# Optimization experiments

Measured on AMD Instinct MI355X. Metric: run time of the kernel, lower is better.

The kernel has to match this reference:

```python
import jax, jax.numpy as jnp
import numpy as np

N, L, S, D, HD, FC = 4, 2048, 2048, 256, 256, 8  # batch, query len, source len, in_depth, hidden_depth, heads
EPS = 1e-12  # F.normalize eps


def setup_inputs() -> dict:
    key = jax.random.key(0)
    ks = jax.random.split(key, 8)
    sc = 0.05
    return {
        "x0": jax.random.normal(ks[0], (N, L, D), jnp.float32),
        "x1": jax.random.normal(ks[1], (N, S, D), jnp.float32),
        "W0": jax.random.normal(ks[2], (D, HD), jnp.float32) * sc,
        "b0": jax.random.normal(ks[3], (HD,), jnp.float32) * sc,
        "W1": jax.random.normal(ks[4], (D, 2 * HD), jnp.float32) * sc,
        "b1": jax.random.normal(ks[5], (2 * HD,), jnp.float32) * sc,
        "Wm": jax.random.normal(ks[6], (HD, D), jnp.float32) * sc,
        "bm": jax.random.normal(ks[7], (D,), jnp.float32) * sc,
        "alpha": jnp.ones((1,), jnp.float32),
        "beta": jnp.zeros((1,), jnp.float32),
    }


def _l2norm(x):
    # F.normalize(dim=2): x / max(||x||, eps)
    return x / jnp.maximum(jnp.linalg.norm(x, axis=2, keepdims=True), EPS)


def reference(x0, x1, W0, b0, W1, b1, Wm, bm, alpha, beta):
    n, l, _ = x0.shape
    s = x1.shape[1]
    fc = FC
    m = n * fc
    # projections + head split: 'n l (fc c) -> (n fc) l c'
    x0p = (x0 @ W0 + b0).reshape(n, l, fc, -1).transpose(0, 2, 1, 3).reshape(m, l, -1)
    x1p = (x1 @ W1 + b1).reshape(n, s, fc, -1).transpose(0, 2, 1, 3).reshape(m, s, -1)
    x1_point, x1_value = jnp.split(x1p, 2, axis=2)  # each (m, s, c)
    # cosine similarity (m, l, s)
    sim = jnp.einsum('mlc,msc->mls', _l2norm(x0p), _l2norm(x1_point))
    sim = jax.nn.sigmoid(alpha * sim + beta)
    max_val = jnp.max(sim, axis=2)              # (m, l)
    max_idx = jnp.argmax(sim, axis=2)           # (m, l)
    gathered = jnp.take_along_axis(x1_value, max_idx[:, :, None], axis=1)  # (m, l, c)
    new_x0 = max_val[:, :, None] * gathered
    # '(n fc) l c -> n l (fc c)'
    new_x0 = new_x0.reshape(n, fc, l, -1).transpose(0, 2, 1, 3).reshape(n, l, -1)
    return new_x0 @ Wm + bm
```

## Files before the change

kernel.cpp:

```cpp
#include <hip/hip_runtime.h>
#include <hip/hip_bf16.h>
#include <cmath>

#define NB   4
#define LQ   2048
#define SK   2048
#define DD   256
#define HD   256
#define FC   8
#define CH   32
#define MHEAD 32

#define MARGIN 0.0085f
#define CAP    12

typedef float f32x16 __attribute__((ext_vector_type(16)));
typedef short bf16x8 __attribute__((ext_vector_type(8)));
typedef unsigned short ushort8v __attribute__((ext_vector_type(8)));

__device__ inline unsigned short f32_to_bf16_bits(float v) {
    __hip_bfloat16 b = __float2bfloat16(v);
    return __builtin_bit_cast(unsigned short, b);
}
__device__ inline unsigned int ord_encode(float v) {
    unsigned int u = __float_as_uint(v);
    return (u & 0x80000000u) ? ~u : (u | 0x80000000u);
}
__device__ inline float ord_decode(unsigned int e) {
    unsigned int u = (e & 0x80000000u) ? (e & 0x7fffffffu) : ~e;
    return __uint_as_float(u);
}

#define MFMA32(a, b, c) __builtin_amdgcn_mfma_f32_32x32x16_bf16(a, b, c, 0, 0, 0)

template<int EPI>
__global__ __launch_bounds__(256)
void gemm_bias_kernel(const float* __restrict__ A, const float* __restrict__ B,
                      const float* __restrict__ bias,
                      float* __restrict__ C0, float* __restrict__ C1,
                      int M, int N, int K)
{
    __shared__ float As[16][68];
    __shared__ float Bs[16][64];
    const int tx = threadIdx.x & 15;
    const int ty = threadIdx.x >> 4;
    const int bm = blockIdx.y * 64;
    const int bn = blockIdx.x * 64;
    float acc[4][4] = {};

    for (int k0 = 0; k0 < K; k0 += 16) {
        {
            const int row = threadIdx.x >> 2;
            const int kq  = (threadIdx.x & 3) << 2;
            const float4 a4 = *(const float4*)&A[(size_t)(bm + row) * K + k0 + kq];
            As[kq + 0][row] = a4.x;
            As[kq + 1][row] = a4.y;
            As[kq + 2][row] = a4.z;
            As[kq + 3][row] = a4.w;
            const int kr = threadIdx.x >> 4;
            const int nq = (threadIdx.x & 15) << 2;
            *(float4*)&Bs[kr][nq] = *(const float4*)&B[(size_t)(k0 + kr) * N + bn + nq];
        }
        __syncthreads();
        #pragma unroll
        for (int kk = 0; kk < 16; ++kk) {
            const float4 a4 = *(const float4*)&As[kk][ty << 2];
            const float4 b4 = *(const float4*)&Bs[kk][tx << 2];
            const float av[4] = {a4.x, a4.y, a4.z, a4.w};
            const float bv[4] = {b4.x, b4.y, b4.z, b4.w};
            #pragma unroll
            for (int i = 0; i < 4; ++i)
                #pragma unroll
                for (int j = 0; j < 4; ++j)
                    acc[i][j] = fmaf(av[i], bv[j], acc[i][j]);
        }
        __syncthreads();
    }

    #pragma unroll
    for (int i = 0; i < 4; ++i) {
        const int row = bm + (ty << 2) + i;
        #pragma unroll
        for (int j = 0; j < 4; ++j) {
            const int col = bn + (tx << 2) + j;
            const float v = acc[i][j] + bias[col];
            if (EPI == 0) {
                C0[(size_t)row * N + col] = v;
            } else if (EPI == 1) {
                const int n = row >> 11, l = row & 2047;
                const int f = col >> 5,  c = col & 31;
                C0[((((size_t)n * FC + f) * LQ) + l) * CH + c] = v;
            } else {
                const int n = row >> 11, s = row & 2047;
                const int f = col >> 6,  c64 = col & 63;
                float* dst = (c64 < CH) ? C0 : C1;
                dst[((((size_t)n * FC + f) * SK) + s) * CH + (c64 & 31)] = v;
            }
        }
    }
}

__global__ __launch_bounds__(256)
void norm_hi_kernel(float* __restrict__ x, unsigned short* __restrict__ dhi,
                    int nrows, const float* __restrict__ alpha)
{
    const int r = blockIdx.x * blockDim.x + threadIdx.x;
    if (r >= nrows) return;
    float* p = x + (size_t)r * CH;
    float4 v[8];
    float ss = 0.f;
    #pragma unroll
    for (int i = 0; i < 8; ++i) {
        v[i] = *(const float4*)(p + i * 4);
        ss = fmaf(v[i].x, v[i].x, ss);
        ss = fmaf(v[i].y, v[i].y, ss);
        ss = fmaf(v[i].z, v[i].z, ss);
        ss = fmaf(v[i].w, v[i].w, ss);
    }
    float sgn = 1.f;
    if (alpha) sgn = (alpha[0] < 0.f) ? -1.f : 1.f;
    const float inv = sgn / fmaxf(sqrtf(ss), 1e-12f);

    ushort8v hb[4];
    #pragma unroll
    for (int i = 0; i < 8; ++i) {
        float4 w;
        w.x = v[i].x * inv; w.y = v[i].y * inv;
        w.z = v[i].z * inv; w.w = v[i].w * inv;
        *(float4*)(p + i * 4) = w;
        hb[i >> 1][(i & 1) * 4 + 0] = f32_to_bf16_bits(w.x);
        hb[i >> 1][(i & 1) * 4 + 1] = f32_to_bf16_bits(w.y);
        hb[i >> 1][(i & 1) * 4 + 2] = f32_to_bf16_bits(w.z);
        hb[i >> 1][(i & 1) * 4 + 3] = f32_to_bf16_bits(w.w);
    }
    #pragma unroll
    for (int i = 0; i < 4; ++i)
        *(ushort8v*)(dhi + (size_t)r * CH + i * 8) = hb[i];
}

__global__ __launch_bounds__(256, 4)
void maxpass_kernel(const unsigned short* __restrict__ qhi,
                    const unsigned short* __restrict__ khi,
                    unsigned int* __restrict__ maxhh_u)
{
    const int b    = blockIdx.x;
    const int sc   = b & 3;
    const int qb   = (b >> 2) & 15;
    const int h    = b >> 6;
    const int wave = threadIdx.x >> 6;
    const int lane = threadIdx.x & 63;
    const int qbase = qb * 128 + wave * 32;
    const int col   = lane & 31;
    const int g8    = (lane >> 5) * 8;

    const size_t qoff = ((size_t)h * LQ + qbase + col) * CH + g8;
    const bf16x8 ah0 = *(const bf16x8*)(qhi + qoff);
    const bf16x8 ah1 = *(const bf16x8*)(qhi + qoff + 16);

    const unsigned short* kh = khi + ((size_t)h * SK + sc * 512) * CH;
    const size_t koff = (size_t)col * CH + g8;

    float maxv[16];
    #pragma unroll
    for (int r = 0; r < 16; ++r) maxv[r] = -INFINITY;

    bf16x8 t0a = *(const bf16x8*)(kh + koff);
    bf16x8 t0b = *(const bf16x8*)(kh + koff + 16);
    bf16x8 t1a = *(const bf16x8*)(kh + koff + 32 * CH);
    bf16x8 t1b = *(const bf16x8*)(kh + koff + 32 * CH + 16);

    for (int sb = 0; sb < 16; sb += 2) {
        const bf16x8 c0a = t0a, c0b = t0b, c1a = t1a, c1b = t1b;
        if (sb + 2 < 16) {
            const size_t o = koff + (size_t)(sb + 2) * 32 * CH;
            t0a = *(const bf16x8*)(kh + o);
            t0b = *(const bf16x8*)(kh + o + 16);
            t1a = *(const bf16x8*)(kh + o + 32 * CH);
            t1b = *(const bf16x8*)(kh + o + 32 * CH + 16);
        }
        f32x16 c = {0.f, 0.f, 0.f, 0.f, 0.f, 0.f, 0.f, 0.f,
                    0.f, 0.f, 0.f, 0.f, 0.f, 0.f, 0.f, 0.f};
        c = MFMA32(ah0, c0a, c);
        c = MFMA32(ah1, c0b, c);
        #pragma unroll
        for (int r = 0; r < 16; ++r) maxv[r] = fmaxf(maxv[r], c[r]);
        f32x16 d = {0.f, 0.f, 0.f, 0.f, 0.f, 0.f, 0.f, 0.f,
                    0.f, 0.f, 0.f, 0.f, 0.f, 0.f, 0.f, 0.f};
        d = MFMA32(ah0, c1a, d);
        d = MFMA32(ah1, c1b, d);
        #pragma unroll
        for (int r = 0; r < 16; ++r) maxv[r] = fmaxf(maxv[r], d[r]);
    }

    #pragma unroll
    for (int r = 0; r < 16; ++r) {
        float v = maxv[r];
        #pragma unroll
        for (int m = 16; m >= 1; m >>= 1)
            v = fmaxf(v, __shfl_xor(v, m, 64));
        maxv[r] = v;
    }
    if (col == 0) {
        const int rbase = h * LQ + qbase + 4 * (lane >> 5);
        #pragma unroll
        for (int r = 0; r < 16; ++r)
            atomicMax(&maxhh_u[rbase + (r & 3) + 8 * (r >> 2)], ord_encode(maxv[r]));
    }
}

__global__ __launch_bounds__(256, 4)
void candpass_kernel(const unsigned short* __restrict__ qhi,
                     const unsigned short* __restrict__ khi,
                     const unsigned int* __restrict__ maxhh_u,
                     int* __restrict__ cnt, int* __restrict__ cand)
{
    const int b    = blockIdx.x;
    const int sc   = b & 3;
    const int qb   = (b >> 2) & 15;
    const int h    = b >> 6;
    const int wave = threadIdx.x >> 6;
    const int lane = threadIdx.x & 63;
    const int qbase = qb * 128 + wave * 32;
    const int col   = lane & 31;
    const int g8    = (lane >> 5) * 8;

    const size_t qoff = ((size_t)h * LQ + qbase + col) * CH + g8;
    const bf16x8 ah0 = *(const bf16x8*)(qhi + qoff);
    const bf16x8 ah1 = *(const bf16x8*)(qhi + qoff + 16);

    int   rows[16];
    float thr[16];
    {
        const int rbase = h * LQ + qbase + 4 * (lane >> 5);
        #pragma unroll
        for (int r = 0; r < 16; ++r) {
            rows[r] = rbase + (r & 3) + 8 * (r >> 2);
            thr[r]  = ord_decode(maxhh_u[rows[r]]) - MARGIN;
        }
    }

    const unsigned short* kh = khi + ((size_t)h * SK + sc * 512) * CH;
    const size_t koff = (size_t)col * CH + g8;
    const int sbase = sc * 512;

    bf16x8 t0a = *(const bf16x8*)(kh + koff);
    bf16x8 t0b = *(const bf16x8*)(kh + koff + 16);
    bf16x8 t1a = *(const bf16x8*)(kh + koff + 32 * CH);
    bf16x8 t1b = *(const bf16x8*)(kh + koff + 32 * CH + 16);

    for (int sb = 0; sb < 16; sb += 2) {
        const bf16x8 c0a = t0a, c0b = t0b, c1a = t1a, c1b = t1b;
        if (sb + 2 < 16) {
            const size_t o = koff + (size_t)(sb + 2) * 32 * CH;
            t0a = *(const bf16x8*)(kh + o);
            t0b = *(const bf16x8*)(kh + o + 16);
            t1a = *(const bf16x8*)(kh + o + 32 * CH);
            t1b = *(const bf16x8*)(kh + o + 32 * CH + 16);
        }
        f32x16 c = {0.f, 0.f, 0.f, 0.f, 0.f, 0.f, 0.f, 0.f,
                    0.f, 0.f, 0.f, 0.f, 0.f, 0.f, 0.f, 0.f};
        c = MFMA32(ah0, c0a, c);
        c = MFMA32(ah1, c0b, c);
        f32x16 d = {0.f, 0.f, 0.f, 0.f, 0.f, 0.f, 0.f, 0.f,
                    0.f, 0.f, 0.f, 0.f, 0.f, 0.f, 0.f, 0.f};
        d = MFMA32(ah0, c1a, d);
        d = MFMA32(ah1, c1b, d);
        const int s0 = sbase + sb * 32 + col;
        #pragma unroll
        for (int r = 0; r < 16; ++r) {
            if (c[r] >= thr[r]) {
                const int slot = atomicAdd(&cnt[rows[r]], 1);
                if (slot < CAP) cand[(size_t)rows[r] * CAP + slot] = s0;
            }
            if (d[r] >= thr[r]) {
                const int slot = atomicAdd(&cnt[rows[r]], 1);
                if (slot < CAP) cand[(size_t)rows[r] * CAP + slot] = s0 + 32;
            }
        }
    }
}

__global__ __launch_bounds__(256)
void refine_gather_kernel(const float* __restrict__ qn,
                          const float* __restrict__ kn,
                          const int* __restrict__ cnt, const int* __restrict__ cand,
                          const float* __restrict__ xv,
                          const float* __restrict__ alpha, const float* __restrict__ beta,
                          unsigned short* __restrict__ nxb)
{
    const int r = blockIdx.x * blockDim.x + threadIdx.x;
    const int h = r >> 11, l = r & 2047;

    float qr[CH];
    #pragma unroll
    for (int i = 0; i < 8; ++i) {
        const float4 v = *(const float4*)(qn + (size_t)r * CH + i * 4);
        qr[i * 4 + 0] = v.x; qr[i * 4 + 1] = v.y;
        qr[i * 4 + 2] = v.z; qr[i * 4 + 3] = v.w;
    }

    int m = cnt[r];
    if (m > CAP) m = CAP;
    float best = -INFINITY;
    int   bidx = 0x7fffffff;
    for (int j = 0; j < m; ++j) {
        const int s = cand[(size_t)r * CAP + j];
        const float4* k4 = (const float4*)(kn + ((size_t)h * SK + s) * CH);
        float p = 0.f;
        #pragma unroll
        for (int c = 0; c < 8; ++c) {
            const float4 kv = k4[c];
            p = fmaf(qr[c * 4 + 0], kv.x, p);
            p = fmaf(qr[c * 4 + 1], kv.y, p);
            p = fmaf(qr[c * 4 + 2], kv.z, p);
            p = fmaf(qr[c * 4 + 3], kv.w, p);
        }
        if (p > best || (p == best && s < bidx)) { best = p; bidx = s; }
    }
    if (bidx == 0x7fffffff) bidx = 0;

    const float a = alpha[0], be = beta[0];
    float tv;
    int idx = bidx;
    if (a == 0.f) { idx = 0; tv = be; }
    else          { tv = fmaf(fabsf(a), best, be); }
    float val;
    if (tv >= 0.f) val = 1.f / (1.f + expf(-tv));
    else           { const float e = expf(tv); val = e / (1.f + e); }

    const float4* vr = (const float4*)(xv + ((size_t)h * SK + idx) * CH);
    const int n = h >> 3, f = h & 7;
    unsigned short* out = nxb + (((size_t)n * LQ + l) * (FC * CH)) + f * CH;
    #pragma unroll
    for (int i = 0; i < 8; ++i) {
        const float4 w = vr[i];
        ushort8v o;
        o[0] = f32_to_bf16_bits(w.x * val);
        o[1] = f32_to_bf16_bits(w.y * val);
        o[2] = f32_to_bf16_bits(w.z * val);
        o[3] = f32_to_bf16_bits(w.w * val);
        *(unsigned long long*)(out + i * 4) = __builtin_bit_cast(unsigned long long,
            *(const ulong1*)&o);
    }
}

__global__ __launch_bounds__(256)
void wmprep_kernel(const float* __restrict__ Wm, unsigned short* __restrict__ wm_s)
{
    const int i = blockIdx.x * 256 + threadIdx.x;
    const int k = i >> 8, n = i & 255;
    wm_s[(k >> 4) * 4096 + n * 16 + (k & 15)] = f32_to_bf16_bits(Wm[k * 256 + n]);
}

__global__ __launch_bounds__(256)
void gemm_out_mfma_kernel(const unsigned short* __restrict__ nxb,
                          const unsigned short* __restrict__ wm_s,
                          const float* __restrict__ bm, float* __restrict__ out)
{
    const int wave = threadIdx.x >> 6;
    const int lane = threadIdx.x & 63;
    const int idx  = blockIdx.x * 4 + wave;
    const int mt   = idx >> 3;
    const int nt   = idx & 7;
    const int col  = lane & 31;
    const int g8   = (lane >> 5) * 8;

    const unsigned short* aptr = nxb + (size_t)(mt * 32 + col) * 256 + g8;
    const unsigned short* bptr = wm_s + nt * 32 * 16 + col * 16 + g8;

    f32x16 acc = {0.f, 0.f, 0.f, 0.f, 0.f, 0.f, 0.f, 0.f,
                  0.f, 0.f, 0.f, 0.f, 0.f, 0.f, 0.f, 0.f};
    #pragma unroll 4
    for (int kc = 0; kc < 16; ++kc) {
        const bf16x8 a = *(const bf16x8*)(aptr + kc * 16);
        const bf16x8 bfr = *(const bf16x8*)(bptr + (size_t)kc * 4096);
        acc = MFMA32(a, bfr, acc);
    }

    const int n0 = nt * 32;
    const float bias = bm[n0 + col];
    #pragma unroll
    for (int r = 0; r < 16; ++r) {
        const int row = mt * 32 + (r & 3) + 8 * (r >> 2) + 4 * (lane >> 5);
        out[(size_t)row * 256 + n0 + col] = acc[r] + bias;
    }
}

extern "C" void kernel_launch(void* const* d_in, const int* in_sizes, int n_in,
                              void* d_out, int out_size, void* d_ws, size_t ws_size,
                              hipStream_t stream)
{
    const float* x0 = (const float*)d_in[0];
    const float* x1 = (const float*)d_in[1];
    const float* W0 = (const float*)d_in[2];
    const float* b0 = (const float*)d_in[3];
    const float* W1 = (const float*)d_in[4];
    const float* b1 = (const float*)d_in[5];
    const float* Wm = (const float*)d_in[6];
    const float* bm = (const float*)d_in[7];
    const float* alpha = (const float*)d_in[8];
    const float* beta  = (const float*)d_in[9];
    float* out = (float*)d_out;

    char* ws = (char*)d_ws;
    const size_t MB = 1024ull * 1024ull;
    float* x0q = (float*)(ws + 0);
    float* x1k = (float*)(ws + 8 * MB);
    float* x1v = (float*)(ws + 16 * MB);
    unsigned short* qhi = (unsigned short*)(ws + 24 * MB);
    unsigned short* khi = (unsigned short*)(ws + 28 * MB);
    unsigned int* maxhh_u = (unsigned int*)(ws + 32 * MB);
    int* cnt  = (int*)(ws + 32 * MB + 256 * 1024);
    int* cand = (int*)(ws + 32 * MB + 512 * 1024);
    unsigned short* wm_s = (unsigned short*)(ws + 32 * MB + 3584 * 1024);
    unsigned short* nxb  = (unsigned short*)(ws + 24 * MB);

    const int Mrows = NB * LQ;

    gemm_bias_kernel<1><<<dim3(HD / 64, Mrows / 64), 256, 0, stream>>>(
        x0, W0, b0, x0q, nullptr, Mrows, HD, DD);
    gemm_bias_kernel<2><<<dim3(2 * HD / 64, Mrows / 64), 256, 0, stream>>>(
        x1, W1, b1, x1k, x1v, Mrows, 2 * HD, DD);
    wmprep_kernel<<<256, 256, 0, stream>>>(Wm, wm_s);
    norm_hi_kernel<<<(MHEAD * LQ) / 256, 256, 0, stream>>>(x0q, qhi, MHEAD * LQ, alpha);
    norm_hi_kernel<<<(MHEAD * SK) / 256, 256, 0, stream>>>(x1k, khi, MHEAD * SK, nullptr);
    hipMemsetAsync(maxhh_u, 0, (size_t)MHEAD * LQ * 4, stream);
    hipMemsetAsync(cnt, 0, (size_t)MHEAD * LQ * 4, stream);
    maxpass_kernel<<<2048, 256, 0, stream>>>(qhi, khi, maxhh_u);
    candpass_kernel<<<2048, 256, 0, stream>>>(qhi, khi, maxhh_u, cnt, cand);
    refine_gather_kernel<<<(MHEAD * LQ) / 256, 256, 0, stream>>>(
        x0q, x1k, cnt, cand, x1v, alpha, beta, nxb);
    gemm_out_mfma_kernel<<<512, 256, 0, stream>>>(nxb, wm_s, bm, out);
}
```

Baseline: 157.7 us.

## Double-buffer projection GEMM tiles and fuse norm kernels with buffer zeroing

The projection GEMM now keeps two shared-memory buffers and register-prefetches the next K chunk while computing the current one, so only one barrier is needed per iteration. Separately, the two norm launches and the two memsets are merged into a single kernel that normalizes both Q and K rows and zeroes the max and count buffers. This is meant to hide global load latency in the GEMM and to cut launch and memset overhead, at the cost of doubled LDS use and more live registers in the GEMM.

Result: faster. 149.9 us (-5.0%).

```diff
diff --git a/kernel.cpp b/kernel.cpp
--- a/kernel.cpp
+++ b/kernel.cpp
@@ -40,32 +40,43 @@
                       float* __restrict__ C0, float* __restrict__ C1,
                       int M, int N, int K)
 {
-    __shared__ float As[16][68];
-    __shared__ float Bs[16][64];
+    __shared__ float As[2][16][68];
+    __shared__ float Bs[2][16][64];
     const int tx = threadIdx.x & 15;
     const int ty = threadIdx.x >> 4;
     const int bm = blockIdx.y * 64;
     const int bn = blockIdx.x * 64;
     float acc[4][4] = {};
 
-    for (int k0 = 0; k0 < K; k0 += 16) {
-        {
-            const int row = threadIdx.x >> 2;
-            const int kq  = (threadIdx.x & 3) << 2;
-            const float4 a4 = *(const float4*)&A[(size_t)(bm + row) * K + k0 + kq];
-            As[kq + 0][row] = a4.x;
-            As[kq + 1][row] = a4.y;
-            As[kq + 2][row] = a4.z;
-            As[kq + 3][row] = a4.w;
-            const int kr = threadIdx.x >> 4;
-            const int nq = (threadIdx.x & 15) << 2;
-            *(float4*)&Bs[kr][nq] = *(const float4*)&B[(size_t)(k0 + kr) * N + bn + nq];
-        }
-        __syncthreads();
+    const int arow = threadIdx.x >> 2;
+    const int akq  = (threadIdx.x & 3) << 2;
+    const int bkr  = threadIdx.x >> 4;
+    const int bnq  = (threadIdx.x & 15) << 2;
+
+    {
+        const float4 a4 = *(const float4*)&A[(size_t)(bm + arow) * K + akq];
+        const float4 b4 = *(const float4*)&B[(size_t)bkr * N + bn + bnq];
+        As[0][akq + 0][arow] = a4.x;
+        As[0][akq + 1][arow] = a4.y;
+        As[0][akq + 2][arow] = a4.z;
+        As[0][akq + 3][arow] = a4.w;
+        *(float4*)&Bs[0][bkr][bnq] = b4;
+    }
+    __syncthreads();
+
+    const int nchunk = K >> 4;
+    float4 pa, pb;
+    for (int c = 0; c < nchunk; ++c) {
+        const int cur = c & 1;
+        if (c + 1 < nchunk) {
+            const int k0 = (c + 1) << 4;
+            pa = *(const float4*)&A[(size_t)(bm + arow) * K + k0 + akq];
+            pb = *(const float4*)&B[(size_t)(k0 + bkr) * N + bn + bnq];
+        }
         #pragma unroll
         for (int kk = 0; kk < 16; ++kk) {
-            const float4 a4 = *(const float4*)&As[kk][ty << 2];
-            const float4 b4 = *(const float4*)&Bs[kk][tx << 2];
+            const float4 a4 = *(const float4*)&As[cur][kk][ty << 2];
+            const float4 b4 = *(const float4*)&Bs[cur][kk][tx << 2];
             const float av[4] = {a4.x, a4.y, a4.z, a4.w};
             const float bv[4] = {b4.x, b4.y, b4.z, b4.w};
             #pragma unroll
@@ -73,6 +84,14 @@
                 #pragma unroll
                 for (int j = 0; j < 4; ++j)
                     acc[i][j] = fmaf(av[i], bv[j], acc[i][j]);
+        }
+        if (c + 1 < nchunk) {
+            const int nxt = cur ^ 1;
+            As[nxt][akq + 0][arow] = pa.x;
+            As[nxt][akq + 1][arow] = pa.y;
+            As[nxt][akq + 2][arow] = pa.z;
+            As[nxt][akq + 3][arow] = pa.w;
+            *(float4*)&Bs[nxt][bkr][bnq] = pb;
         }
         __syncthreads();
     }
@@ -101,12 +120,27 @@
 }
 
 __global__ __launch_bounds__(256)
-void norm_hi_kernel(float* __restrict__ x, unsigned short* __restrict__ dhi,
-                    int nrows, const float* __restrict__ alpha)
-{
-    const int r = blockIdx.x * blockDim.x + threadIdx.x;
-    if (r >= nrows) return;
-    float* p = x + (size_t)r * CH;
+void norm_split_init_kernel(float* __restrict__ xq, unsigned short* __restrict__ qhi,
+                            float* __restrict__ xk, unsigned short* __restrict__ khi,
+                            const float* __restrict__ alpha,
+                            unsigned int* __restrict__ maxhh_u, int* __restrict__ cnt)
+{
+    int r = blockIdx.x * blockDim.x + threadIdx.x;
+    float* p;
+    unsigned short* dhi;
+    float sgn = 1.f;
+    if (r < MHEAD * LQ) {
+        maxhh_u[r] = 0u;
+        cnt[r] = 0;
+        p   = xq + (size_t)r * CH;
+        dhi = qhi + (size_t)r * CH;
+        if (alpha[0] < 0.f) sgn = -1.f;
+    } else {
+        r -= MHEAD * LQ;
+        p   = xk + (size_t)r * CH;
+        dhi = khi + (size_t)r * CH;
+    }
+
     float4 v[8];
     float ss = 0.f;
     #pragma unroll
@@ -117,8 +151,6 @@
         ss = fmaf(v[i].z, v[i].z, ss);
         ss = fmaf(v[i].w, v[i].w, ss);
     }
-    float sgn = 1.f;
-    if (alpha) sgn = (alpha[0] < 0.f) ? -1.f : 1.f;
     const float inv = sgn / fmaxf(sqrtf(ss), 1e-12f);
 
     ushort8v hb[4];
@@ -135,7 +167,7 @@
     }
     #pragma unroll
     for (int i = 0; i < 4; ++i)
-        *(ushort8v*)(dhi + (size_t)r * CH + i * 8) = hb[i];
+        *(ushort8v*)(dhi + i * 8) = hb[i];
 }
 
 __global__ __launch_bounds__(256, 4)
@@ -422,10 +454,8 @@
     gemm_bias_kernel<2><<<dim3(2 * HD / 64, Mrows / 64), 256, 0, stream>>>(
         x1, W1, b1, x1k, x1v, Mrows, 2 * HD, DD);
     wmprep_kernel<<<256, 256, 0, stream>>>(Wm, wm_s);
-    norm_hi_kernel<<<(MHEAD * LQ) / 256, 256, 0, stream>>>(x0q, qhi, MHEAD * LQ, alpha);
-    norm_hi_kernel<<<(MHEAD * SK) / 256, 256, 0, stream>>>(x1k, khi, MHEAD * SK, nullptr);
-    hipMemsetAsync(maxhh_u, 0, (size_t)MHEAD * LQ * 4, stream);
-    hipMemsetAsync(cnt, 0, (size_t)MHEAD * LQ * 4, stream);
+    norm_split_init_kernel<<<(2 * MHEAD * LQ) / 256, 256, 0, stream>>>(
+        x0q, qhi, x1k, khi, alpha, maxhh_u, cnt);
     maxpass_kernel<<<2048, 256, 0, stream>>>(qhi, khi, maxhh_u);
     candpass_kernel<<<2048, 256, 0, stream>>>(qhi, khi, maxhh_u, cnt, cand);
     refine_gather_kernel<<<(MHEAD * LQ) / 256, 256, 0, stream>>>(
```
